# Kernel optimization log

Hardware: AMD Instinct MI355X
Metric: run time of the kernel (lower is better)

The kernel has to match this reference:

```python
import jax, jax.numpy as jnp
import numpy as np

HIDDEN_DIM = 2048
NUM_HEADS = 16
HEAD_DIM = HIDDEN_DIM // NUM_HEADS


def setup_inputs() -> dict:
    key = jax.random.key(0)
    k1, k2, k3 = jax.random.split(key, 3)
    x = jax.random.normal(k1, (2, 2048, HIDDEN_DIM), dtype=jnp.float32)
    # nn.Linear weight layout is [out, in]; we store transposed [in, out] for x @ W
    W_qkv = jax.random.normal(k2, (HIDDEN_DIM, 3 * HIDDEN_DIM), dtype=jnp.float32) * (HIDDEN_DIM ** -0.5)
    W_out = jax.random.normal(k3, (HIDDEN_DIM, HIDDEN_DIM), dtype=jnp.float32) * (HIDDEN_DIM ** -0.5)
    return {"x": x, "W_qkv": W_qkv, "W_out": W_out}


def reference(x, W_qkv, W_out):
    B, T, D = x.shape
    H, Hd = NUM_HEADS, HEAD_DIM
    qkv = (x @ W_qkv).reshape(B, T, 3, H, Hd)
    q = qkv[:, :, 0].transpose(0, 2, 1, 3)  # [B,H,T,Hd]
    k = qkv[:, :, 1].transpose(0, 2, 1, 3)
    v = qkv[:, :, 2].transpose(0, 2, 1, 3)
    scale = 1.0 / jnp.sqrt(jnp.asarray(Hd, dtype=x.dtype))
    attn = jnp.einsum('bhqd,bhkd->bhqk', q, k) * scale  # [B,H,T,T]
    causal = jnp.tril(jnp.ones((T, T), dtype=bool))
    attn = jnp.where(causal, attn, jnp.asarray(-jnp.inf, dtype=attn.dtype))
    attn = jax.nn.softmax(attn, axis=-1)
    out = jnp.einsum('bhqk,bhkd->bhqd', attn, v)  # [B,H,T,Hd]
    out = out.transpose(0, 2, 1, 3).reshape(B, T, D)
    return out @ W_out
```

## Files before the change

### kernel.cpp

```cpp
#include <hip/hip_runtime.h>


typedef unsigned short ushort;
typedef __attribute__((ext_vector_type(8))) short short8;
typedef __attribute__((ext_vector_type(4))) float floatx4;

#define T_SEQ 2048
#define NQKV  6144
#define DMODEL 2048
#define HDIM  128
#define NEG_BIG (-3.0e38f)

#define WAITVM(n) asm volatile("s_waitcnt vmcnt(" #n ")" ::: "memory")
#define WAITLGKM0 asm volatile("s_waitcnt lgkmcnt(0)" ::: "memory")

__device__ __forceinline__ ushort f2bf(float f) {
  unsigned u = __float_as_uint(f);
  u += 0x7fffu + ((u >> 16) & 1u);
  return (ushort)(u >> 16);
}
__device__ __forceinline__ void stout(ushort* p, float v) { *p = f2bf(v); }
__device__ __forceinline__ void stout(float* p, float v)  { *p = v; }

__device__ __forceinline__ void gload_lds16(const ushort* g, ushort* l) {
  __builtin_amdgcn_global_load_lds(
      (const __attribute__((address_space(1))) void*)g,
      (__attribute__((address_space(3))) void*)l,
      16, 0, 0);
}

__global__ void cvt2d(const float* __restrict__ in, ushort* __restrict__ out,
                      int R, int C, int ld_in) {
  int idx = blockIdx.x * blockDim.x + threadIdx.x;
  int c4 = C >> 2;
  if (idx >= R * c4) return;
  int r = idx / c4, c = (idx - r * c4) * 4;
  float4 v = *(const float4*)(in + (size_t)r * ld_in + c);
  ushort4 o;
  o.x = f2bf(v.x); o.y = f2bf(v.y); o.z = f2bf(v.z); o.w = f2bf(v.w);
  *(ushort4*)(out + (size_t)r * C + c) = o;
}

__global__ void cvt2dT(const float* __restrict__ in, ushort* __restrict__ out,
                       int R, int C, int ld_in) {
  __shared__ float tile[32][33];
  int c0 = blockIdx.x * 32, r0 = blockIdx.y * 32;
  int tx = threadIdx.x, ty = threadIdx.y;
#pragma unroll
  for (int q = 0; q < 4; q++)
    tile[ty + q * 8][tx] = in[(size_t)(r0 + ty + q * 8) * ld_in + c0 + tx];
  __syncthreads();
#pragma unroll
  for (int q = 0; q < 4; q++)
    out[(size_t)(c0 + ty + q * 8) * R + r0 + tx] = f2bf(tile[tx][ty + q * 8]);
}

template <typename OutT>
__global__ void gemm_bt(
    const ushort* __restrict__ A, const ushort* __restrict__ Bt,
    OutT* __restrict__ C, int M, int N, int K, int ldc) {
  __shared__ ushort sA[128 * 32];
  __shared__ ushort sB[128 * 32];
  const int tid = threadIdx.x;
  const int w = tid >> 6, l = tid & 63;
  const int quad = l >> 4, l16 = l & 15;
  const int row0 = blockIdx.x * 128, col0 = blockIdx.y * 128;
  const int wm = (w >> 1) * 64, wn = (w & 1) * 64;

  floatx4 acc[4][4];
  const floatx4 zero = {0.f, 0.f, 0.f, 0.f};
#pragma unroll
  for (int i = 0; i < 4; i++)
#pragma unroll
    for (int j = 0; j < 4; j++) acc[i][j] = zero;

  const int srow = w * 16 + (l >> 2);
  const int scol = (l & 3) * 8;
  const ushort* gA = A + (size_t)(row0 + srow) * K + scol;
  const ushort* gB = Bt + (size_t)(col0 + srow) * K + scol;
  ushort* lA = &sA[(w * 16) * 32];
  ushort* lB = &sB[(w * 16) * 32];

  for (int k0 = 0; k0 < K; k0 += 32) {
    __syncthreads();
    gload_lds16(gA + k0, lA);
    gload_lds16(gA + k0 + (size_t)64 * K, lA + 64 * 32);
    gload_lds16(gB + k0, lB);
    gload_lds16(gB + k0 + (size_t)64 * K, lB + 64 * 32);
    __syncthreads();
    short8 af[4], bfr[4];
#pragma unroll
    for (int i = 0; i < 4; i++)
      af[i] = *(const short8*)&sA[(wm + i * 16 + l16) * 32 + quad * 8];
#pragma unroll
    for (int j = 0; j < 4; j++)
      bfr[j] = *(const short8*)&sB[(wn + j * 16 + l16) * 32 + quad * 8];
#pragma unroll
    for (int i = 0; i < 4; i++)
#pragma unroll
      for (int j = 0; j < 4; j++)
        acc[i][j] = __builtin_amdgcn_mfma_f32_16x16x32_bf16(af[i], bfr[j], acc[i][j], 0, 0, 0);
  }

#pragma unroll
  for (int i = 0; i < 4; i++)
#pragma unroll
    for (int j = 0; j < 4; j++) {
      int r0 = row0 + wm + i * 16 + quad * 4;
      int c = col0 + wn + j * 16 + l16;
#pragma unroll
      for (int r = 0; r < 4; r++)
        stout(&C[(size_t)(r0 + r) * ldc + c], acc[i][j][r]);
    }
}

template <typename OutT>
__global__ __launch_bounds__(512, 2) void gemm_qkv(
    const ushort* __restrict__ A, const ushort* __restrict__ Bt,
    OutT* __restrict__ C, int M, int N, int K, int ldc) {
  __shared__ ushort sA[3][256 * 32];
  __shared__ ushort sB[3][384 * 32];
  const int tid = threadIdx.x;
  const int wid = tid >> 6, l = tid & 63;
  const int quad = l >> 4, l16 = l & 15;
  const int wr = wid >> 2, wc = wid & 3;
  const int row0 = blockIdx.x * 256, col0 = blockIdx.y * 384;
  const int NT = K >> 5;

  floatx4 acc[8][6];
  const floatx4 zero = {0.f, 0.f, 0.f, 0.f};
#pragma unroll
  for (int i = 0; i < 8; i++)
#pragma unroll
    for (int j = 0; j < 6; j++) acc[i][j] = zero;

  const int sgr = ((l & 3) ^ ((l >> 3) & 3)) * 8;
  const ushort* gA = A + (size_t)(row0 + wid * 32 + (l >> 2)) * K + sgr;
  const ushort* gB = Bt + (size_t)(col0 + wid * 48 + (l >> 2)) * K + sgr;

  auto stageA = [&](int tt) {
    ushort* dst = &sA[tt % 3][(wid * 32) * 32];
    const ushort* g = gA + tt * 32;
    gload_lds16(g, dst);
    gload_lds16(g + (size_t)16 * K, dst + 16 * 32);
  };
  auto stageB = [&](int tt) {
    ushort* dst = &sB[tt % 3][(wid * 48) * 32];
    const ushort* g = gB + tt * 32;
    gload_lds16(g, dst);
    gload_lds16(g + (size_t)16 * K, dst + 16 * 32);
    gload_lds16(g + (size_t)32 * K, dst + 32 * 32);
  };

  const int gsw = (quad ^ ((l16 >> 1) & 3)) * 8;

  stageA(0); stageB(0);
  if (NT > 1) {
    stageA(1); stageB(1);
    WAITVM(5);
  } else {
    WAITVM(0);
  }
  __builtin_amdgcn_s_barrier();

  for (int t = 0; t < NT; ++t) {
    const int b = t % 3;
    short8 af[4], bfr[6];
#pragma unroll
    for (int j = 0; j < 6; j++)
      bfr[j] = *(const short8*)&sB[b][(wc * 96 + j * 16 + l16) * 32 + gsw];
#pragma unroll
    for (int i = 0; i < 4; i++)
      af[i] = *(const short8*)&sA[b][(wr * 128 + i * 16 + l16) * 32 + gsw];
    if (t + 2 < NT) stageA(t + 2);
    __builtin_amdgcn_s_barrier();
    WAITLGKM0;
    __builtin_amdgcn_s_setprio(1);
#pragma unroll
    for (int i = 0; i < 4; i++)
#pragma unroll
      for (int j = 0; j < 6; j++)
        acc[i][j] = __builtin_amdgcn_mfma_f32_16x16x32_bf16(af[i], bfr[j], acc[i][j], 0, 0, 0);
    __builtin_amdgcn_s_setprio(0);
    __builtin_amdgcn_s_barrier();
#pragma unroll
    for (int i = 0; i < 4; i++)
      af[i] = *(const short8*)&sA[b][(wr * 128 + (4 + i) * 16 + l16) * 32 + gsw];
    if (t + 2 < NT) stageB(t + 2);
    __builtin_amdgcn_s_barrier();
    WAITLGKM0;
    __builtin_amdgcn_s_setprio(1);
#pragma unroll
    for (int i = 0; i < 4; i++)
#pragma unroll
      for (int j = 0; j < 6; j++)
        acc[4 + i][j] = __builtin_amdgcn_mfma_f32_16x16x32_bf16(af[i], bfr[j], acc[4 + i][j], 0, 0, 0);
    __builtin_amdgcn_s_setprio(0);
    if (t < NT - 2) { WAITVM(5); } else if (t == NT - 2) { WAITVM(0); }
    __builtin_amdgcn_s_barrier();
  }

#pragma unroll
  for (int mi = 0; mi < 8; mi++)
#pragma unroll
    for (int j = 0; j < 6; j++) {
      int r0 = row0 + wr * 128 + mi * 16 + quad * 4;
      int c = col0 + wc * 96 + j * 16 + l16;
#pragma unroll
      for (int r = 0; r < 4; r++)
        stout(&C[(size_t)(r0 + r) * ldc + c], acc[mi][j][r]);
    }
}

__global__ __launch_bounds__(256, 2) void flash_attn(
    const ushort* __restrict__ qkv, ushort* __restrict__ attn) {
  __shared__ ushort sK[2][16 * 528];
  __shared__ ushort sVt[128 * 72];
  __shared__ ushort sP[4 * 16 * 72];

  const int tid = threadIdx.x;
  const int w = tid >> 6, l = tid & 63;
  const int quad = l >> 4, l16 = l & 15;
  const int bh = blockIdx.x;
  const int qt = 31 - (int)blockIdx.y;
  const int b = bh >> 4, h = bh & 15;
  const size_t rowbase = (size_t)b * T_SEQ;

  short8 qf[4];
  {
    const ushort* qp = qkv + (rowbase + qt * 64 + w * 16 + l16) * NQKV + h * HDIM + quad * 8;
#pragma unroll
    for (int s = 0; s < 4; s++) qf[s] = *(const short8*)(qp + s * 32);
  }
  floatx4 o[8];
  const floatx4 zero = {0.f, 0.f, 0.f, 0.f};
#pragma unroll
  for (int n = 0; n < 8; n++) o[n] = zero;
  float m_i[4], l_i[4];
#pragma unroll
  for (int r = 0; r < 4; r++) { m_i[r] = NEG_BIG; l_i[r] = 0.f; }

  const ushort* gK = qkv + (rowbase + w * 16 + (l >> 4)) * NQKV + 2048 + h * HDIM + (l & 15) * 8;
  auto issueK = [&](int kt, int buf) {
#pragma unroll
    for (int c = 0; c < 4; c++)
      gload_lds16(gK + (size_t)(kt * 64 + c * 4) * NQKV, &sK[buf][(w * 4 + c) * 528]);
  };
  const int v_hd0 = (tid & 15) * 8;
  const int v_t0 = 2 * (tid >> 4);
  const ushort* gV = qkv + rowbase * NQKV + 4096 + h * HDIM + v_hd0;
  short8 vcur[4], vnxt[4];
  auto loadV = [&](int kt, short8* dst) {
#pragma unroll
    for (int c = 0; c < 2; c++) {
      const ushort* g = gV + (size_t)(kt * 64 + v_t0 + 32 * c) * NQKV;
      dst[c] = *(const short8*)g;
      dst[2 + c] = *(const short8*)(g + NQKV);
    }
  };

  ushort* myP = &sP[w * 16 * 72];
  const float scale = 0.08838834764831845f;

  auto attn_step = [&](bool diag, int buf) {
    floatx4 S[4];
#pragma unroll
    for (int j = 0; j < 4; j++) S[j] = zero;
#pragma unroll
    for (int s = 0; s < 4; s++)
#pragma unroll
      for (int j = 0; j < 4; j++) {
        int row = j * 16 + l16;
        short8 kf = *(const short8*)&sK[buf][(row >> 2) * 528 + (row & 3) * 128 + s * 32 + quad * 8];
        S[j] = __builtin_amdgcn_mfma_f32_16x16x32_bf16(qf[s], kf, S[j], 0, 0, 0);
      }
#pragma unroll
    for (int j = 0; j < 4; j++)
#pragma unroll
      for (int r = 0; r < 4; r++) {
        float v = S[j][r] * scale;
        if (diag && (j * 16 + l16 > w * 16 + quad * 4 + r)) v = NEG_BIG;
        S[j][r] = v;
      }
    float alpha[4];
#pragma unroll
    for (int r = 0; r < 4; r++) {
      float v = fmaxf(fmaxf(S[0][r], S[1][r]), fmaxf(S[2][r], S[3][r]));
      v = fmaxf(v, __shfl_xor(v, 1, 16));
      v = fmaxf(v, __shfl_xor(v, 2, 16));
      v = fmaxf(v, __shfl_xor(v, 4, 16));
      v = fmaxf(v, __shfl_xor(v, 8, 16));
      float mn = fmaxf(m_i[r], v);
      alpha[r] = __expf(m_i[r] - mn);
      m_i[r] = mn;
    }
#pragma unroll
    for (int j = 0; j < 4; j++)
#pragma unroll
      for (int r = 0; r < 4; r++) S[j][r] = __expf(S[j][r] - m_i[r]);
#pragma unroll
    for (int r = 0; r < 4; r++)
      l_i[r] = l_i[r] * alpha[r] + S[0][r] + S[1][r] + S[2][r] + S[3][r];
#pragma unroll
    for (int n = 0; n < 8; n++)
#pragma unroll
      for (int r = 0; r < 4; r++) o[n][r] *= alpha[r];
#pragma unroll
    for (int j = 0; j < 4; j++)
#pragma unroll
      for (int r = 0; r < 4; r++)
        myP[(quad * 4 + r) * 72 + j * 16 + l16] = f2bf(S[j][r]);
#pragma unroll
    for (int s = 0; s < 2; s++) {
      short8 pf = *(const short8*)&myP[l16 * 72 + s * 32 + quad * 8];
#pragma unroll
      for (int n = 0; n < 8; n++) {
        int hd = n * 16 + l16;
        short8 vf = *(const short8*)&sVt[hd * 72 + 8 * ((s * 4 + quad) ^ ((hd >> 3) & 7))];
        o[n] = __builtin_amdgcn_mfma_f32_16x16x32_bf16(pf, vf, o[n], 0, 0, 0);
      }
    }
  };

  issueK(0, 0);
  loadV(0, vcur);
  for (int kt = 0; kt <= qt; kt++) {
    const int buf = kt & 1;
    __syncthreads();
#pragma unroll
    for (int c = 0; c < 2; c++) {
      int tw = (v_t0 >> 1) + 16 * c;
#pragma unroll
      for (int j = 0; j < 8; j++) {
        int hd = v_hd0 + j;
        int phys = hd * 72 + 2 * (tw & 3) + 8 * ((tw >> 2) ^ ((hd >> 3) & 7));
        unsigned pv = ((unsigned)(ushort)vcur[c][j]) | (((unsigned)(ushort)vcur[2 + c][j]) << 16);
        *(unsigned*)&sVt[phys] = pv;
      }
    }
    __syncthreads();
    if (kt < qt) {
      issueK(kt + 1, buf ^ 1);
      loadV(kt + 1, vnxt);
    }
    attn_step(kt == qt, buf);
    if (kt < qt) {
#pragma unroll
      for (int c = 0; c < 4; c++) vcur[c] = vnxt[c];
    }
  }

#pragma unroll
  for (int r = 0; r < 4; r++) {
    float v = l_i[r];
    v += __shfl_xor(v, 1, 16);
    v += __shfl_xor(v, 2, 16);
    v += __shfl_xor(v, 4, 16);
    v += __shfl_xor(v, 8, 16);
    l_i[r] = 1.0f / v;
  }
#pragma unroll
  for (int n = 0; n < 8; n++) {
    int col = h * HDIM + n * 16 + l16;
#pragma unroll
    for (int r = 0; r < 4; r++) {
      int row = qt * 64 + w * 16 + quad * 4 + r;
      attn[(rowbase + row) * DMODEL + col] = f2bf(o[n][r] * l_i[r]);
    }
  }
}

extern "C" void kernel_launch(void* const* d_in, const int* in_sizes, int n_in,
                              void* d_out, int out_size, void* d_ws, size_t ws_size,
                              hipStream_t stream) {
  const float* xf    = (const float*)d_in[0];
  const float* Wqkvf = (const float*)d_in[1];
  const float* Woutf = (const float*)d_in[2];
  float* outf = (float*)d_out;
  char* ws = (char*)d_ws;

  const size_t SZ_QKV  = (size_t)4096 * 6144 * 2;
  const size_t SZ_ATTN = (size_t)4096 * 2048 * 2;
  const size_t SZ_WQT  = (size_t)6144 * 2048 * 2;

  ushort* xb = (ushort*)d_out;
  cvt2d<<<8192, 256, 0, stream>>>(xf, xb, 4096, 2048, 2048);

  if (ws_size >= SZ_QKV + SZ_ATTN + SZ_WQT) {
    ushort* qkv   = (ushort*)ws;
    ushort* attnb = (ushort*)(ws + SZ_QKV);
    ushort* WT    = (ushort*)(ws + SZ_QKV + SZ_ATTN);
    cvt2dT<<<dim3(192, 64), dim3(32, 8), 0, stream>>>(Wqkvf, WT, 2048, 6144, NQKV);
    gemm_qkv<ushort><<<dim3(16, 16), 512, 0, stream>>>(xb, WT, qkv, 4096, 6144, 2048, NQKV);
    flash_attn<<<dim3(32, 32), 256, 0, stream>>>(qkv, attnb);
    cvt2dT<<<dim3(64, 64), dim3(32, 8), 0, stream>>>(Woutf, WT, 2048, 2048, 2048);
    gemm_bt<float><<<dim3(32, 16), 256, 0, stream>>>(attnb, WT, outf, 4096, 2048, 2048, DMODEL);
  } else {
    ushort* qkv   = (ushort*)ws;
    float*  of    = (float*)ws;
    ushort* wbT   = (ushort*)d_out + (size_t)4096 * 2048;
    ushort* attnb = xb;
    for (int s = 0; s < 3; s++) {
      cvt2dT<<<dim3(64, 64), dim3(32, 8), 0, stream>>>(Wqkvf + s * 2048, wbT, 2048, 2048, NQKV);
      gemm_bt<ushort><<<dim3(32, 16), 256, 0, stream>>>(xb, wbT, qkv + s * 2048, 4096, 2048, 2048, NQKV);
    }
    flash_attn<<<dim3(32, 32), 256, 0, stream>>>(qkv, attnb);
    cvt2dT<<<dim3(64, 64), dim3(32, 8), 0, stream>>>(Woutf, wbT, 2048, 2048, 2048);
    gemm_bt<float><<<dim3(32, 16), 256, 0, stream>>>(attnb, wbT, of, 4096, 2048, 2048, DMODEL);
    hipMemcpyAsync(outf, of, (size_t)4096 * 2048 * 4, hipMemcpyDeviceToDevice, stream);
  }
}
```

Before: 453.1 us.

## Reshape QKV GEMM to 256x192 tiles with K=64 double-buffered stages

Shrinks the QKV GEMM output tile from 256x384 to 256x192 and doubles the grid to 512 blocks, so more blocks are available to cover the GPU's compute units. The K loop now steps 64 per iteration as two 32-wide sub-stages with double buffering, instead of a 3-deep ring of 32-wide stages. Each sub-stage loads all 8 A fragments and 3 B fragments before issuing MFMAs. The smaller tile halves accumulator registers but lowers arithmetic intensity per loaded byte, and the B loads are now uneven across waves (waves 4-7 load one row group instead of two).

```diff
diff --git a/kernel.cpp b/kernel.cpp
--- a/kernel.cpp
+++ b/kernel.cpp
@@ -118,94 +118,97 @@
 __global__ __launch_bounds__(512, 2) void gemm_qkv(
     const ushort* __restrict__ A, const ushort* __restrict__ Bt,
     OutT* __restrict__ C, int M, int N, int K, int ldc) {
-  __shared__ ushort sA[3][256 * 32];
-  __shared__ ushort sB[3][384 * 32];
+  __shared__ ushort sA[2][2][256 * 32];
+  __shared__ ushort sB[2][2][192 * 32];
   const int tid = threadIdx.x;
   const int wid = tid >> 6, l = tid & 63;
   const int quad = l >> 4, l16 = l & 15;
   const int wr = wid >> 2, wc = wid & 3;
-  const int row0 = blockIdx.x * 256, col0 = blockIdx.y * 384;
-  const int NT = K >> 5;
-
-  floatx4 acc[8][6];
+  const int row0 = blockIdx.x * 256, col0 = blockIdx.y * 192;
+  const int NT = K >> 6;
+
+  floatx4 acc[8][3];
   const floatx4 zero = {0.f, 0.f, 0.f, 0.f};
 #pragma unroll
   for (int i = 0; i < 8; i++)
 #pragma unroll
-    for (int j = 0; j < 6; j++) acc[i][j] = zero;
+    for (int j = 0; j < 3; j++) acc[i][j] = zero;
 
   const int sgr = ((l & 3) ^ ((l >> 3) & 3)) * 8;
   const ushort* gA = A + (size_t)(row0 + wid * 32 + (l >> 2)) * K + sgr;
-  const ushort* gB = Bt + (size_t)(col0 + wid * 48 + (l >> 2)) * K + sgr;
-
-  auto stageA = [&](int tt) {
-    ushort* dst = &sA[tt % 3][(wid * 32) * 32];
-    const ushort* g = gA + tt * 32;
+  const int brow0 = (wid < 4) ? wid * 32 : 128 + (wid - 4) * 16;
+  const ushort* gB = Bt + (size_t)(col0 + brow0 + (l >> 2)) * K + sgr;
+
+  auto stageA = [&](int tt, int ks) {
+    ushort* dst = &sA[tt & 1][ks][(wid * 32) * 32];
+    const ushort* g = gA + tt * 64 + ks * 32;
     gload_lds16(g, dst);
     gload_lds16(g + (size_t)16 * K, dst + 16 * 32);
   };
-  auto stageB = [&](int tt) {
-    ushort* dst = &sB[tt % 3][(wid * 48) * 32];
-    const ushort* g = gB + tt * 32;
+  auto stageB = [&](int tt, int ks) {
+    ushort* dst = &sB[tt & 1][ks][brow0 * 32];
+    const ushort* g = gB + tt * 64 + ks * 32;
     gload_lds16(g, dst);
-    gload_lds16(g + (size_t)16 * K, dst + 16 * 32);
-    gload_lds16(g + (size_t)32 * K, dst + 32 * 32);
+    if (wid < 4) gload_lds16(g + (size_t)16 * K, dst + 16 * 32);
   };
 
   const int gsw = (quad ^ ((l16 >> 1) & 3)) * 8;
 
-  stageA(0); stageB(0);
+  stageA(0, 0); stageB(0, 0); stageA(0, 1); stageB(0, 1);
   if (NT > 1) {
-    stageA(1); stageB(1);
-    WAITVM(5);
+    stageA(1, 0); stageB(1, 0);
+    WAITVM(3);
   } else {
     WAITVM(0);
   }
   __builtin_amdgcn_s_barrier();
 
   for (int t = 0; t < NT; ++t) {
-    const int b = t % 3;
-    short8 af[4], bfr[6];
-#pragma unroll
-    for (int j = 0; j < 6; j++)
-      bfr[j] = *(const short8*)&sB[b][(wc * 96 + j * 16 + l16) * 32 + gsw];
-#pragma unroll
-    for (int i = 0; i < 4; i++)
-      af[i] = *(const short8*)&sA[b][(wr * 128 + i * 16 + l16) * 32 + gsw];
-    if (t + 2 < NT) stageA(t + 2);
+    const int b = t & 1;
+    short8 af[8], bfr[3];
+#pragma unroll
+    for (int j = 0; j < 3; j++)
+      bfr[j] = *(const short8*)&sB[b][0][(wc * 48 + j * 16 + l16) * 32 + gsw];
+#pragma unroll
+    for (int i = 0; i < 8; i++)
+      af[i] = *(const short8*)&sA[b][0][(wr * 128 + i * 16 + l16) * 32 + gsw];
+    if (t + 1 < NT) { stageA(t + 1, 1); stageB(t + 1, 1); }
     __builtin_amdgcn_s_barrier();
     WAITLGKM0;
     __builtin_amdgcn_s_setprio(1);
 #pragma unroll
-    for (int i = 0; i < 4; i++)
-#pragma unroll
-      for (int j = 0; j < 6; j++)
+    for (int i = 0; i < 8; i++)
+#pragma unroll
+      for (int j = 0; j < 3; j++)
         acc[i][j] = __builtin_amdgcn_mfma_f32_16x16x32_bf16(af[i], bfr[j], acc[i][j], 0, 0, 0);
     __builtin_amdgcn_s_setprio(0);
     __builtin_amdgcn_s_barrier();
 #pragma unroll
-    for (int i = 0; i < 4; i++)
-      af[i] = *(const short8*)&sA[b][(wr * 128 + (4 + i) * 16 + l16) * 32 + gsw];
-    if (t + 2 < NT) stageB(t + 2);
+    for (int j = 0; j < 3; j++)
+      bfr[j] = *(const short8*)&sB[b][1][(wc * 48 + j * 16 + l16) * 32 + gsw];
+#pragma unroll
+    for (int i = 0; i < 8; i++)
+      af[i] = *(const short8*)&sA[b][1][(wr * 128 + i * 16 + l16) * 32 + gsw];
+    if (t + 2 < NT) { stageA(t + 2, 0); stageB(t + 2, 0); }
     __builtin_amdgcn_s_barrier();
     WAITLGKM0;
     __builtin_amdgcn_s_setprio(1);
 #pragma unroll
-    for (int i = 0; i < 4; i++)
-#pragma unroll
-      for (int j = 0; j < 6; j++)
-        acc[4 + i][j] = __builtin_amdgcn_mfma_f32_16x16x32_bf16(af[i], bfr[j], acc[4 + i][j], 0, 0, 0);
+    for (int i = 0; i < 8; i++)
+#pragma unroll
+      for (int j = 0; j < 3; j++)
+        acc[i][j] = __builtin_amdgcn_mfma_f32_16x16x32_bf16(af[i], bfr[j], acc[i][j], 0, 0, 0);
     __builtin_amdgcn_s_setprio(0);
-    if (t < NT - 2) { WAITVM(5); } else if (t == NT - 2) { WAITVM(0); }
+    if (t < NT - 2) { WAITVM(3); } else { WAITVM(0); }
     __builtin_amdgcn_s_barrier();
   }
 
 #pragma unroll
   for (int mi = 0; mi < 8; mi++)
 #pragma unroll
-    for (int j = 0; j < 6; j++) {
+    for (int j = 0; j < 3; j++) {
       int r0 = row0 + wr * 128 + mi * 16 + quad * 4;
-      int c = col0 + wc * 96 + j * 16 + l16;
+      int c = col0 + wc * 48 + j * 16 + l16;
 #pragma unroll
       for (int r = 0; r < 4; r++)
         stout(&C[(size_t)(r0 + r) * ldc + c], acc[mi][j][r]);
@@ -391,7 +394,7 @@
     ushort* attnb = (ushort*)(ws + SZ_QKV);
     ushort* WT    = (ushort*)(ws + SZ_QKV + SZ_ATTN);
     cvt2dT<<<dim3(192, 64), dim3(32, 8), 0, stream>>>(Wqkvf, WT, 2048, 6144, NQKV);
-    gemm_qkv<ushort><<<dim3(16, 16), 512, 0, stream>>>(xb, WT, qkv, 4096, 6144, 2048, NQKV);
+    gemm_qkv<ushort><<<dim3(16, 32), 512, 0, stream>>>(xb, WT, qkv, 4096, 6144, 2048, NQKV);
     flash_attn<<<dim3(32, 32), 256, 0, stream>>>(qkv, attnb);
     cvt2dT<<<dim3(64, 64), dim3(32, 8), 0, stream>>>(Woutf, WT, 2048, 2048, 2048);
     gemm_bt<float><<<dim3(32, 16), 256, 0, stream>>>(attnb, WT, outf, 4096, 2048, 2048, DMODEL);
```

Result: faster. 377.2 us (-16.8%).
